# Kernel tuning notes

Measured on AMD Instinct MI355X. Metric: run time of the kernel, lower is better.

Reference implementation:

```python
import jax, jax.numpy as jnp
import numpy as np

B, S, D_IN, D_OUT = 4, 2048, 1024, 1024

def setup_inputs() -> dict:
    key = jax.random.key(0)
    k_x, k_q, k_k, k_v = jax.random.split(key, 4)
    return {
        "x": jax.random.normal(k_x, (B, S, D_IN), dtype=jnp.float32),
        "W_query": jax.random.uniform(k_q, (D_IN, D_OUT), dtype=jnp.float32),
        "W_key": jax.random.uniform(k_k, (D_IN, D_OUT), dtype=jnp.float32),
        "W_value": jax.random.uniform(k_v, (D_IN, D_OUT), dtype=jnp.float32),
    }

def reference(x, W_query, W_key, W_value):
    seq_len = x.shape[1]
    d_out = W_key.shape[-1]
    # fused QKV projection: x @ concat([Wq, Wk, Wv], -1), then split
    qkv = x @ jnp.concatenate([W_query, W_key, W_value], axis=-1)  # [B,S,3*d_out]
    query, key, value = jnp.split(qkv, 3, axis=2)
    # raw scores [B,S,S]; causal mask applied BEFORE scaling (as in source)
    attn_weights = jnp.einsum("bqd,bkd->bqk", query, key)
    causal = jnp.triu(jnp.ones((seq_len, seq_len), dtype=bool), k=1)
    attn_weights = jnp.where(causal[None, :, :], -jnp.inf, attn_weights)
    scaled = attn_weights / jnp.asarray(d_out, x.dtype) ** 0.5
    attn_scores = jax.nn.softmax(scaled, axis=-1)  # dropout p=0 -> identity
    context_vectors = jnp.einsum("bqk,bkd->bqd", attn_scores, value)
    return (context_vectors, attn_scores)
```

## Files before the change

kernel.cpp:

```cpp
#include <hip/hip_runtime.h>
#include <cstdint>
#include <cstddef>


#define S_LEN 2048
#define D_DIM 1024
#define NBATCH 4
#define MEG (1024 * 1024)

typedef __attribute__((ext_vector_type(4))) float floatx4;
typedef __attribute__((ext_vector_type(8))) __bf16 bf16x8;
typedef __attribute__((ext_vector_type(8))) short short8v;

__device__ __forceinline__ unsigned short f2bf(float f) {
  union { float f; unsigned u; } v; v.f = f;
  unsigned r = v.u + 0x7FFF + ((v.u >> 16) & 1);
  return (unsigned short)(r >> 16);
}
__device__ __forceinline__ float bf2f(unsigned short h) {
  union { unsigned u; float f; } v; v.u = ((unsigned)h) << 16; return v.f;
}

__device__ __forceinline__ void async_copy16(const void* g, void* l) {
  __builtin_amdgcn_global_load_lds(
      (const __attribute__((address_space(1))) void*)g,
      (__attribute__((address_space(3))) void*)l, 16, 0, 0);
}

#define VMCNT0() asm volatile("s_waitcnt vmcnt(0)" ::: "memory")
#define RAW_BAR() __builtin_amdgcn_s_barrier()
#define MFMA_BF16 __builtin_amdgcn_mfma_f32_16x16x32_bf16


__device__ __forceinline__ void split_core8(
    const short* __restrict__ Ah, const short* __restrict__ Al,
    const short* __restrict__ Bh, const short* __restrict__ Bl,
    int lda, int ldb, int kIters, int blockM, int blockN,
    short (*AsH)[256][32], short (*AsL)[256][32],
    short (*BsH)[128][32], short (*BsL)[128][32],
    floatx4 (&acc)[4][4])
{
  const int tid  = threadIdx.x;
  const int lane = tid & 63;
  const int wave = tid >> 6;
  const int wm = (wave >> 1) * 64;
  const int wn = (wave & 1) * 64;
  const int fm = lane & 15;
  const int fu = lane >> 4;

  int rA[4], sA[4], rB[4], sB[4];
  #pragma unroll
  for (int i = 0; i < 4; ++i) {
    rA[i] = wm + i * 16 + fm;
    sA[i] = (fu ^ ((rA[i] >> 1) & 3)) * 8;
    rB[i] = wn + i * 16 + fm;
    sB[i] = (fu ^ ((rB[i] >> 1) & 3)) * 8;
  }

  floatx4 zero = {0.f, 0.f, 0.f, 0.f};
  #pragma unroll
  for (int i = 0; i < 4; ++i)
    #pragma unroll
    for (int j = 0; j < 4; ++j)
      acc[i][j] = zero;

  const int r0 = tid >> 2;
  const int u0 = tid & 3;
  const int su = (u0 ^ ((r0 >> 1) & 3)) * 8;
  const size_t a0 = (size_t)(blockM + r0) * lda + su;
  const size_t a1 = a0 + (size_t)128 * lda;
  const size_t b0 = (size_t)(blockN + r0) * ldb + su;

  auto stage0 = [&](int bf, int kb) {
    async_copy16(Ah + a0 + kb, &AsH[bf][r0][u0 * 8]);
    async_copy16(Al + a0 + kb, &AsL[bf][r0][u0 * 8]);
    async_copy16(Bh + b0 + kb, &BsH[bf][r0][u0 * 8]);
  };
  auto stage1 = [&](int bf, int kb) {
    async_copy16(Ah + a1 + kb, &AsH[bf][r0 + 128][u0 * 8]);
    async_copy16(Al + a1 + kb, &AsL[bf][r0 + 128][u0 * 8]);
    async_copy16(Bl + b0 + kb, &BsL[bf][r0][u0 * 8]);
  };

  stage0(0, 0);
  stage1(0, 0);
  VMCNT0();
  RAW_BAR();

  for (int kt = 0; kt < kIters; ++kt) {
    const int cur = kt & 1;
    const int kb = (kt + 1) * 32;
    const bool pf = (kt + 1) < kIters;

    bf16x8 bh[4], bl[4];
    #pragma unroll
    for (int j = 0; j < 4; ++j) {
      bh[j] = *(const bf16x8*)(&BsH[cur][rB[j]][sB[j]]);
      bl[j] = *(const bf16x8*)(&BsL[cur][rB[j]][sB[j]]);
    }
    bf16x8 ah0 = *(const bf16x8*)(&AsH[cur][rA[0]][sA[0]]);
    bf16x8 al0 = *(const bf16x8*)(&AsL[cur][rA[0]][sA[0]]);
    bf16x8 ah1 = *(const bf16x8*)(&AsH[cur][rA[1]][sA[1]]);
    bf16x8 al1 = *(const bf16x8*)(&AsL[cur][rA[1]][sA[1]]);
    if (pf) stage0(cur ^ 1, kb);
    RAW_BAR();
    __builtin_amdgcn_s_setprio(1);
    #pragma unroll
    for (int j = 0; j < 4; ++j) {
      acc[0][j] = MFMA_BF16(ah0, bh[j], acc[0][j], 0, 0, 0);
      acc[0][j] = MFMA_BF16(ah0, bl[j], acc[0][j], 0, 0, 0);
      acc[0][j] = MFMA_BF16(al0, bh[j], acc[0][j], 0, 0, 0);
      acc[1][j] = MFMA_BF16(ah1, bh[j], acc[1][j], 0, 0, 0);
      acc[1][j] = MFMA_BF16(ah1, bl[j], acc[1][j], 0, 0, 0);
      acc[1][j] = MFMA_BF16(al1, bh[j], acc[1][j], 0, 0, 0);
    }
    __builtin_amdgcn_s_setprio(0);
    RAW_BAR();

    bf16x8 ah2 = *(const bf16x8*)(&AsH[cur][rA[2]][sA[2]]);
    bf16x8 al2 = *(const bf16x8*)(&AsL[cur][rA[2]][sA[2]]);
    bf16x8 ah3 = *(const bf16x8*)(&AsH[cur][rA[3]][sA[3]]);
    bf16x8 al3 = *(const bf16x8*)(&AsL[cur][rA[3]][sA[3]]);
    if (pf) stage1(cur ^ 1, kb);
    RAW_BAR();
    __builtin_amdgcn_s_setprio(1);
    #pragma unroll
    for (int j = 0; j < 4; ++j) {
      acc[2][j] = MFMA_BF16(ah2, bh[j], acc[2][j], 0, 0, 0);
      acc[2][j] = MFMA_BF16(ah2, bl[j], acc[2][j], 0, 0, 0);
      acc[2][j] = MFMA_BF16(al2, bh[j], acc[2][j], 0, 0, 0);
      acc[3][j] = MFMA_BF16(ah3, bh[j], acc[3][j], 0, 0, 0);
      acc[3][j] = MFMA_BF16(ah3, bl[j], acc[3][j], 0, 0, 0);
      acc[3][j] = MFMA_BF16(al3, bh[j], acc[3][j], 0, 0, 0);
    }
    __builtin_amdgcn_s_setprio(0);
    VMCNT0();
    RAW_BAR();
  }
}

__device__ __forceinline__ void single_core8(
    const short* __restrict__ A, const short* __restrict__ B,
    int lda, int ldb, int kIters, int blockM, int blockN,
    short (*As)[256][32], short (*Bs)[128][32], floatx4 (&acc)[4][4])
{
  const int tid  = threadIdx.x;
  const int lane = tid & 63;
  const int wave = tid >> 6;
  const int wm = (wave >> 1) * 64;
  const int wn = (wave & 1) * 64;
  const int fm = lane & 15;
  const int fu = lane >> 4;

  int rA[4], sA[4], rB[4], sB[4];
  #pragma unroll
  for (int i = 0; i < 4; ++i) {
    rA[i] = wm + i * 16 + fm;
    sA[i] = (fu ^ ((rA[i] >> 1) & 3)) * 8;
    rB[i] = wn + i * 16 + fm;
    sB[i] = (fu ^ ((rB[i] >> 1) & 3)) * 8;
  }

  floatx4 zero = {0.f, 0.f, 0.f, 0.f};
  #pragma unroll
  for (int i = 0; i < 4; ++i)
    #pragma unroll
    for (int j = 0; j < 4; ++j)
      acc[i][j] = zero;

  const int r0 = tid >> 2;
  const int u0 = tid & 3;
  const int su = (u0 ^ ((r0 >> 1) & 3)) * 8;
  const size_t a0 = (size_t)(blockM + r0) * lda + su;
  const size_t a1 = a0 + (size_t)128 * lda;
  const size_t b0 = (size_t)(blockN + r0) * ldb + su;

  auto stage0 = [&](int bf, int kb) {
    async_copy16(A + a0 + kb, &As[bf][r0][u0 * 8]);
    async_copy16(B + b0 + kb, &Bs[bf][r0][u0 * 8]);
  };
  auto stage1 = [&](int bf, int kb) {
    async_copy16(A + a1 + kb, &As[bf][r0 + 128][u0 * 8]);
  };

  stage0(0, 0);
  stage1(0, 0);
  VMCNT0();
  RAW_BAR();

  for (int kt = 0; kt < kIters; ++kt) {
    const int cur = kt & 1;
    const int kb = (kt + 1) * 32;
    const bool pf = (kt + 1) < kIters;

    bf16x8 bfr[4];
    #pragma unroll
    for (int j = 0; j < 4; ++j)
      bfr[j] = *(const bf16x8*)(&Bs[cur][rB[j]][sB[j]]);
    bf16x8 a0f = *(const bf16x8*)(&As[cur][rA[0]][sA[0]]);
    bf16x8 a1f = *(const bf16x8*)(&As[cur][rA[1]][sA[1]]);
    if (pf) stage0(cur ^ 1, kb);
    RAW_BAR();
    __builtin_amdgcn_s_setprio(1);
    #pragma unroll
    for (int j = 0; j < 4; ++j) {
      acc[0][j] = MFMA_BF16(a0f, bfr[j], acc[0][j], 0, 0, 0);
      acc[1][j] = MFMA_BF16(a1f, bfr[j], acc[1][j], 0, 0, 0);
    }
    __builtin_amdgcn_s_setprio(0);
    RAW_BAR();

    bf16x8 a2f = *(const bf16x8*)(&As[cur][rA[2]][sA[2]]);
    bf16x8 a3f = *(const bf16x8*)(&As[cur][rA[3]][sA[3]]);
    if (pf) stage1(cur ^ 1, kb);
    RAW_BAR();
    __builtin_amdgcn_s_setprio(1);
    #pragma unroll
    for (int j = 0; j < 4; ++j) {
      acc[2][j] = MFMA_BF16(a2f, bfr[j], acc[2][j], 0, 0, 0);
      acc[3][j] = MFMA_BF16(a3f, bfr[j], acc[3][j], 0, 0, 0);
    }
    __builtin_amdgcn_s_setprio(0);
    VMCNT0();
    RAW_BAR();
  }
}


__global__ __launch_bounds__(256) void k_cvt_w(
    const float* __restrict__ wq, const float* __restrict__ wk,
    const float* __restrict__ wv,
    short* __restrict__ wqh, short* __restrict__ wql,
    short* __restrict__ wkh, short* __restrict__ wkl,
    short* __restrict__ wvt, float* __restrict__ muSum,
    int* __restrict__ cnt)
{
  const int bid = blockIdx.x;
  const int tid = threadIdx.x;
  if (bid < 1024) {
    const float4* src;
    short *dh, *dl;
    size_t idx;
    if (bid < 512) {
      idx = (size_t)bid * 256 + tid;
      src = (const float4*)wq; dh = wqh; dl = wql;
    } else {
      idx = (size_t)(bid - 512) * 256 + tid;
      src = (const float4*)wk; dh = wkh; dl = wkl;
    }
    const float4 u4 = src[idx * 2];
    const float4 w4 = src[idx * 2 + 1];
    float f[8] = {u4.x, u4.y, u4.z, u4.w, w4.x, w4.y, w4.z, w4.w};
    short8v oh, ol;
    #pragma unroll
    for (int e = 0; e < 8; ++e) {
      const unsigned short h = f2bf(f[e]);
      oh[e] = (short)h;
      ol[e] = (short)f2bf(f[e] - bf2f(h));
    }
    *(short8v*)(dh + idx * 8) = oh;
    *(short8v*)(dl + idx * 8) = ol;
  } else {
    if (bid == 1024) {
      float4 z = {0.f, 0.f, 0.f, 0.f};
      ((float4*)muSum)[tid] = z;
      if (tid == 0) *cnt = 0;
    }
    const int rem = bid - 1024;
    const int bx = rem & 31, by = rem >> 5;
    const int tx = tid & 31, ty = tid >> 5;
    __shared__ float tile[32][33];
    const int colIn = bx * 32 + tx;
    #pragma unroll
    for (int i = 0; i < 4; ++i) {
      const int rowIn = by * 32 + ty + i * 8;
      tile[ty + i * 8][tx] = wv[(size_t)rowIn * D_DIM + colIn];
    }
    __syncthreads();
    const int colOut = by * 32 + tx;
    #pragma unroll
    for (int i = 0; i < 4; ++i) {
      const int rowOut = bx * 32 + ty + i * 8;
      wvt[(size_t)rowOut * D_DIM + colOut] = (short)f2bf(tile[tx][ty + i * 8]);
    }
  }
}


__global__ __launch_bounds__(256) void k_m_cvtx(
    const short* __restrict__ wqh, const short* __restrict__ wql,
    const short* __restrict__ wkh, const short* __restrict__ wkl,
    short* __restrict__ mth, short* __restrict__ mtl,
    float* __restrict__ muSum,
    const float4* __restrict__ x,
    short* __restrict__ xh, short* __restrict__ xl)
{
  __shared__ alignas(16) short AsH[2][64][32];
  __shared__ alignas(16) short AsL[2][64][32];
  __shared__ alignas(16) short BsH[2][64][32];
  __shared__ alignas(16) short BsL[2][64][32];
  const int g = blockIdx.x;
  const int tid = threadIdx.x;

  if (g < 256) {
    floatx4 acc[2][2];
    const int blockM = (g >> 4) * 64;
    const int blockN = (g & 15) * 64;
    const int lane = tid & 63, wave = tid >> 6;
    const int wm = (wave >> 1) * 32, wn = (wave & 1) * 32;
    const int fm = lane & 15, fk = (lane >> 4) * 8;

    floatx4 zero = {0.f, 0.f, 0.f, 0.f};
    #pragma unroll
    for (int i = 0; i < 2; ++i)
      #pragma unroll
      for (int j = 0; j < 2; ++j)
        acc[i][j] = zero;

    const int sr = tid >> 2;
    const int sc = (tid & 3) * 8;
    const short* ah0 = wkh + (size_t)(blockM + sr) * D_DIM + sc;
    const short* al0 = wkl + (size_t)(blockM + sr) * D_DIM + sc;
    const short* bh0 = wqh + (size_t)(blockN + sr) * D_DIM + sc;
    const short* bl0 = wql + (size_t)(blockN + sr) * D_DIM + sc;
    short* ahB = &AsH[0][0][0]; short* alB = &AsL[0][0][0];
    short* bhB = &BsH[0][0][0]; short* blB = &BsL[0][0][0];
    const int l0 = tid * 8, l1 = (tid + 256) * 8;

    for (int kt = 0; kt < 16; ++kt) {
      const int kb = kt * 64;
      async_copy16(ah0 + kb, ahB + l0);
      async_copy16(ah0 + kb + 32, ahB + l1);
      async_copy16(al0 + kb, alB + l0);
      async_copy16(al0 + kb + 32, alB + l1);
      async_copy16(bh0 + kb, bhB + l0);
      async_copy16(bh0 + kb + 32, bhB + l1);
      async_copy16(bl0 + kb, blB + l0);
      async_copy16(bl0 + kb + 32, blB + l1);
      __syncthreads();
      #pragma unroll
      for (int ks = 0; ks < 2; ++ks) {
        bf16x8 ah[2], al[2], bh[2], bl[2];
        #pragma unroll
        for (int i = 0; i < 2; ++i) {
          ah[i] = *(const bf16x8*)(&AsH[ks][wm + i * 16 + fm][fk]);
          al[i] = *(const bf16x8*)(&AsL[ks][wm + i * 16 + fm][fk]);
        }
        #pragma unroll
        for (int j = 0; j < 2; ++j) {
          bh[j] = *(const bf16x8*)(&BsH[ks][wn + j * 16 + fm][fk]);
          bl[j] = *(const bf16x8*)(&BsL[ks][wn + j * 16 + fm][fk]);
        }
        #pragma unroll
        for (int i = 0; i < 2; ++i)
          #pragma unroll
          for (int j = 0; j < 2; ++j) {
            acc[i][j] = MFMA_BF16(ah[i], bh[j], acc[i][j], 0, 0, 0);
            acc[i][j] = MFMA_BF16(ah[i], bl[j], acc[i][j], 0, 0, 0);
            acc[i][j] = MFMA_BF16(al[i], bh[j], acc[i][j], 0, 0, 0);
          }
      }
      __syncthreads();
    }

    const int rb = wm + ((lane >> 4) << 2);
    const int cb = wn + (lane & 15);
    #pragma unroll
    for (int i = 0; i < 2; ++i)
      #pragma unroll
      for (int j = 0; j < 2; ++j) {
        const int n = blockN + cb + j * 16;
        #pragma unroll
        for (int r = 0; r < 2 * 2; ++r) {
          const int m = blockM + rb + i * 16 + r;
          const float f = acc[i][j][r];
          const unsigned short h = f2bf(f);
          mth[(size_t)m * D_DIM + n] = (short)h;
          mtl[(size_t)m * D_DIM + n] = (short)f2bf(f - bf2f(h));
        }
      }
    #pragma unroll
    for (int i = 0; i < 2; ++i)
      #pragma unroll
      for (int r = 0; r < 4; ++r) {
        float v = acc[i][0][r] + acc[i][1][r];
        v += __shfl_xor(v, 1); v += __shfl_xor(v, 2);
        v += __shfl_xor(v, 4); v += __shfl_xor(v, 8);
        if ((lane & 15) == 0)
          atomicAdd(&muSum[blockM + rb + i * 16 + r], v);
      }
  } else {
    const size_t idx = (size_t)(g - 256) * 256 + tid;
    const float4 u4 = x[idx * 2];
    const float4 w4 = x[idx * 2 + 1];
    float f[8] = {u4.x, u4.y, u4.z, u4.w, w4.x, w4.y, w4.z, w4.w};
    short8v oh, ol;
    #pragma unroll
    for (int e = 0; e < 8; ++e) {
      const unsigned short h = f2bf(f[e]);
      oh[e] = (short)h;
      ol[e] = (short)f2bf(f[e] - bf2f(h));
    }
    *(short8v*)(xh + idx * 8) = oh;
    *(short8v*)(xl + idx * 8) = ol;
  }
}


__global__ __launch_bounds__(256) void k_rowstats(
    const short* __restrict__ xh, const short* __restrict__ xl,
    const float* __restrict__ muSum, float* __restrict__ sq, float* __restrict__ u)
{
  const int r = blockIdx.x, tid = threadIdx.x;
  const ushort4 h = *(const ushort4*)(xh + (size_t)r * D_DIM + tid * 4);
  const ushort4 l = *(const ushort4*)(xl + (size_t)r * D_DIM + tid * 4);
  const float4 m4 = *(const float4*)(muSum + tid * 4);
  const float x0 = bf2f(h.x) + bf2f(l.x);
  const float x1 = bf2f(h.y) + bf2f(l.y);
  const float x2 = bf2f(h.z) + bf2f(l.z);
  const float x3 = bf2f(h.w) + bf2f(l.w);
  float s = x0 + x1 + x2 + x3;
  float uu = m4.x * x0 + m4.y * x1 + m4.z * x2 + m4.w * x3;
  #pragma unroll
  for (int off = 32; off > 0; off >>= 1) {
    s  += __shfl_xor(s, off);
    uu += __shfl_xor(uu, off);
  }
  __shared__ float ps[4], pu[4];
  if ((tid & 63) == 0) { ps[tid >> 6] = s; pu[tid >> 6] = uu; }
  __syncthreads();
  if (tid == 0) {
    sq[r] = ps[0] + ps[1] + ps[2] + ps[3];
    u[r]  = (pu[0] + pu[1] + pu[2] + pu[3]) * (1.0f / 1024.0f);
  }
}


__global__ __launch_bounds__(512) void k_gemm_n8(
    const short* __restrict__ xh, const short* __restrict__ xl,
    const short* __restrict__ mth, const short* __restrict__ mtl,
    const float* __restrict__ sq, const float* __restrict__ muSum,
    short* __restrict__ nh, short* __restrict__ nl)
{
  __shared__ alignas(16) short AsH[2][256][32];
  __shared__ alignas(16) short AsL[2][256][32];
  __shared__ alignas(16) short BsH[2][128][32];
  __shared__ alignas(16) short BsL[2][128][32];
  floatx4 acc[4][4];
  const int g = blockIdx.x;
  const int swz = (g & 7) * 32 + (g >> 3);
  const int blockM = (swz >> 3) * 256;
  const int blockN = (swz & 7) * 128;
  split_core8(xh, xl, mth, mtl, D_DIM, D_DIM, D_DIM / 32,
              blockM, blockN, AsH, AsL, BsH, BsL, acc);

  const int tid = threadIdx.x, lane = tid & 63, wave = tid >> 6;
  const int wm = (wave >> 1) * 64, wn = (wave & 1) * 64;
  const int rb = wm + ((lane >> 4) << 2);
  const int cb = wn + (lane & 15);
  #pragma unroll
  for (int i = 0; i < 4; ++i)
    #pragma unroll
    for (int j = 0; j < 4; ++j) {
      const int n = blockN + cb + j * 16;
      const float muv = muSum[n] * (1.0f / 1024.0f);
      #pragma unroll
      for (int r = 0; r < 4; ++r) {
        const int m = blockM + rb + i * 16 + r;
        const float f = acc[i][j][r] - sq[m] * muv;
        const unsigned short h = f2bf(f);
        nh[(size_t)m * D_DIM + n] = (short)h;
        nl[(size_t)m * D_DIM + n] = (short)f2bf(f - bf2f(h));
      }
    }
}


__global__ __launch_bounds__(512) void k_gemm_sv8(
    const short* __restrict__ nh, const short* __restrict__ nl,
    const short* __restrict__ xh, const short* __restrict__ xl,
    const float* __restrict__ sq, const float* __restrict__ u,
    const short* __restrict__ wvt, float* __restrict__ attn,
    short* __restrict__ vt, int* __restrict__ cnt)
{
  __shared__ alignas(16) short AsH[2][256][32];
  __shared__ alignas(16) short AsL[2][256][32];
  __shared__ alignas(16) short BsH[2][128][32];
  __shared__ alignas(16) short BsL[2][128][32];
  __shared__ int s_item;

  const int tid = threadIdx.x, lane = tid & 63, wave = tid >> 6;
  const int wm = (wave >> 1) * 64, wn = (wave & 1) * 64;
  const int rb = wm + ((lane >> 4) << 2);
  const int cb = wn + (lane & 15);

  for (;;) {
    if (tid == 0) s_item = atomicAdd(cnt, 1);
    __syncthreads();
    const int item = s_item;
    if (item >= 544) return;

    floatx4 acc[4][4];
    if (item < 288) {
      const int b = item / 72;
      int t = item - b * 72;
      int bi = 0;
      while (t >= 2 * bi + 2) { t -= 2 * bi + 2; ++bi; }
      const int bj = t;

      const size_t boff = (size_t)b * S_LEN * D_DIM;
      split_core8(nh + boff, nl + boff, xh + boff, xl + boff,
                  D_DIM, D_DIM, D_DIM / 32, bi * 256, bj * 128,
                  AsH, AsL, BsH, BsL, acc);

      float* out = attn + (size_t)b * S_LEN * S_LEN;
      const int rowBase = (b << 11) + bi * 256;
      const int colBase = (b << 11) + bj * 128;
      #pragma unroll
      for (int j = 0; j < 4; ++j) {
        const int n = bj * 128 + cb + j * 16;
        const float uv = u[colBase + cb + j * 16];
        #pragma unroll
        for (int i = 0; i < 4; ++i)
          #pragma unroll
          for (int r = 0; r < 4; ++r) {
            const int m = bi * 256 + rb + i * 16 + r;
            const float sv = sq[rowBase + rb + i * 16 + r];
            out[(size_t)m * S_LEN + n] = acc[i][j][r] + sv * uv;
          }
      }
    } else {
      const int vb = item - 288;
      const int blockM = (vb >> 3) * 256;
      const int blockN = (vb & 7) * 128;
      single_core8(xh, wvt, D_DIM, D_DIM, D_DIM / 32, blockM, blockN,
                   AsH, BsH, acc);
      #pragma unroll
      for (int i = 0; i < 4; ++i)
        #pragma unroll
        for (int j = 0; j < 4; ++j) {
          const int n = blockN + cb + j * 16;
          const int m0 = blockM + rb + i * 16;
          const int b = m0 >> 11;
          const int s0 = m0 & (S_LEN - 1);
          ushort4 pk;
          pk.x = f2bf(acc[i][j][0]); pk.y = f2bf(acc[i][j][1]);
          pk.z = f2bf(acc[i][j][2]); pk.w = f2bf(acc[i][j][3]);
          *(ushort4*)(vt + ((size_t)b * D_DIM + n) * S_LEN + s0) = pk;
        }
    }
  }
}


__global__ __launch_bounds__(256) void k_softmax(float* __restrict__ attn,
                                                 short* __restrict__ pb) {
  const int b = blockIdx.x >> 11;
  const int q = blockIdx.x & (S_LEN - 1);
  float* row  = attn + ((size_t)b * S_LEN + q) * S_LEN;
  short* prow = pb   + ((size_t)b * S_LEN + q) * S_LEN;
  const int tid = threadIdx.x;
  const int k0 = tid * 8;
  const int kBand = ((q >> 7) + 1) << 7;
  __shared__ float sMax[4], sSum[4];

  float v[8];
  if (k0 <= q) {
    const float4 a0 = *(const float4*)(row + k0);
    const float4 a1 = *(const float4*)(row + k0 + 4);
    v[0] = a0.x; v[1] = a0.y; v[2] = a0.z; v[3] = a0.w;
    v[4] = a1.x; v[5] = a1.y; v[6] = a1.z; v[7] = a1.w;
  } else {
    #pragma unroll
    for (int e = 0; e < 8; ++e) v[e] = -3.0e38f;
  }

  float mx = -3.0e38f;
  #pragma unroll
  for (int e = 0; e < 8; ++e) {
    v[e] = (k0 + e <= q) ? v[e] : -3.0e38f;
    mx = fmaxf(mx, v[e]);
  }
  #pragma unroll
  for (int off = 32; off > 0; off >>= 1) mx = fmaxf(mx, __shfl_xor(mx, off));
  if ((tid & 63) == 0) sMax[tid >> 6] = mx;
  __syncthreads();
  mx = fmaxf(fmaxf(sMax[0], sMax[1]), fmaxf(sMax[2], sMax[3]));

  float s = 0.f;
  #pragma unroll
  for (int e = 0; e < 8; ++e) {
    const float p = (k0 + e <= q) ? __expf((v[e] - mx) * 0.03125f) : 0.f;
    v[e] = p;
    s += p;
  }
  #pragma unroll
  for (int off = 32; off > 0; off >>= 1) s += __shfl_xor(s, off);
  if ((tid & 63) == 0) sSum[tid >> 6] = s;
  __syncthreads();
  s = sSum[0] + sSum[1] + sSum[2] + sSum[3];
  const float inv = 1.0f / s;

  float o[8];
  #pragma unroll
  for (int e = 0; e < 8; ++e) o[e] = v[e] * inv;
  float4 w0 = {o[0], o[1], o[2], o[3]};
  float4 w1 = {o[4], o[5], o[6], o[7]};
  *(float4*)(row + k0) = w0;
  *(float4*)(row + k0 + 4) = w1;
  if (k0 < kBand) {
    ushort4 p0, p1;
    p0.x = f2bf(o[0]); p0.y = f2bf(o[1]); p0.z = f2bf(o[2]); p0.w = f2bf(o[3]);
    p1.x = f2bf(o[4]); p1.y = f2bf(o[5]); p1.z = f2bf(o[6]); p1.w = f2bf(o[7]);
    *(ushort4*)(prow + k0) = p0;
    *(ushort4*)(prow + k0 + 4) = p1;
  }
}


__global__ __launch_bounds__(256) void k_gemm_ctx(
    const short* __restrict__ pb, const short* __restrict__ vt,
    float* __restrict__ ctx)
{
  __shared__ alignas(16) short As2[2][128][32];
  __shared__ alignas(16) short Bs2[2][128][32];
  floatx4 acc[4][4];
  const int b = blockIdx.z;
  const int by = 15 - blockIdx.y;
  const int blockM = by * 128;
  const int blockN = blockIdx.x * 128;
  const int kIters = (by + 1) * 2;
  const short* A = pb + (size_t)b * S_LEN * S_LEN;
  const short* B = vt + (size_t)b * D_DIM * S_LEN;

  const int tid = threadIdx.x, lane = tid & 63, wave = tid >> 6;
  const int wm = (wave >> 1) * 64, wn = (wave & 1) * 64;
  const int fm = lane & 15, fk = (lane >> 4) * 8;
  const int r0 = tid >> 2, c0 = (tid & 3) * 8;

  floatx4 zero = {0.f, 0.f, 0.f, 0.f};
  #pragma unroll
  for (int i = 0; i < 4; ++i)
    #pragma unroll
    for (int j = 0; j < 4; ++j)
      acc[i][j] = zero;

  const short* a0 = A + (size_t)(blockM + r0) * S_LEN + c0;
  const short* a1 = a0 + (size_t)64 * S_LEN;
  const short* b0 = B + (size_t)(blockN + r0) * S_LEN + c0;
  const short* b1 = b0 + (size_t)64 * S_LEN;
  short* asBase = &As2[0][0][0];
  short* bsBase = &Bs2[0][0][0];
  short* as0 = asBase + (size_t)tid * 8;
  short* as1 = asBase + (size_t)(tid + 256) * 8;
  short* as2 = asBase + (size_t)(tid + 512) * 8;
  short* as3 = asBase + (size_t)(tid + 768) * 8;
  short* bs0 = bsBase + (size_t)tid * 8;
  short* bs1 = bsBase + (size_t)(tid + 256) * 8;
  short* bs2 = bsBase + (size_t)(tid + 512) * 8;
  short* bs3 = bsBase + (size_t)(tid + 768) * 8;

  for (int kt = 0; kt < kIters; ++kt) {
    const int kb = kt * 64;
    async_copy16(a0 + kb, as0);
    async_copy16(a1 + kb, as1);
    async_copy16(a0 + kb + 32, as2);
    async_copy16(a1 + kb + 32, as3);
    async_copy16(b0 + kb, bs0);
    async_copy16(b1 + kb, bs1);
    async_copy16(b0 + kb + 32, bs2);
    async_copy16(b1 + kb + 32, bs3);
    __syncthreads();
    #pragma unroll
    for (int ks = 0; ks < 2; ++ks) {
      bf16x8 af[4], bfr[4];
      #pragma unroll
      for (int i = 0; i < 4; ++i)
        af[i] = *(const bf16x8*)(&As2[ks][wm + i * 16 + fm][fk]);
      #pragma unroll
      for (int j = 0; j < 4; ++j)
        bfr[j] = *(const bf16x8*)(&Bs2[ks][wn + j * 16 + fm][fk]);
      #pragma unroll
      for (int i = 0; i < 4; ++i)
        #pragma unroll
        for (int j = 0; j < 4; ++j)
          acc[i][j] = MFMA_BF16(af[i], bfr[j], acc[i][j], 0, 0, 0);
    }
    __syncthreads();
  }

  float* out = ctx + (size_t)b * S_LEN * D_DIM;
  const int rb = wm + ((lane >> 4) << 2);
  const int cb = wn + (lane & 15);
  #pragma unroll
  for (int i = 0; i < 4; ++i)
    #pragma unroll
    for (int j = 0; j < 4; ++j) {
      const int n = blockN + cb + j * 16;
      #pragma unroll
      for (int r = 0; r < 4; ++r) {
        const int m = blockM + rb + i * 16 + r;
        out[(size_t)m * D_DIM + n] = acc[i][j][r];
      }
    }
}


extern "C" void kernel_launch(void* const* d_in, const int* in_sizes, int n_in,
                              void* d_out, int out_size, void* d_ws, size_t ws_size,
                              hipStream_t stream) {
  const float* x  = (const float*)d_in[0];
  const float* wq = (const float*)d_in[1];
  const float* wk = (const float*)d_in[2];
  const float* wv = (const float*)d_in[3];

  float* out  = (float*)d_out;
  float* ctx  = out;
  float* attn = out + (size_t)NBATCH * S_LEN * D_DIM;

  short* ws  = (short*)d_ws;
  short* xh  = ws;
  short* xl  = xh + (size_t)8 * MEG;
  short* wqh = xl + (size_t)8 * MEG;
  short* wql = wqh + (size_t)1 * MEG;
  short* wkh = wql + (size_t)1 * MEG;
  short* wkl = wkh + (size_t)1 * MEG;
  short* wvt = wkl + (size_t)1 * MEG;
  short* mth = wvt + (size_t)1 * MEG;
  short* mtl = mth + (size_t)1 * MEG;
  short* nh  = mtl + (size_t)1 * MEG;
  short* nl  = nh + (size_t)8 * MEG;
  short* vt  = nl + (size_t)8 * MEG;
  short* pb  = nh;
  float* fb  = (float*)(vt + (size_t)8 * MEG);
  float* muS = fb;
  float* sq  = fb + 1024;
  float* u   = sq + 8192;
  int*   cnt = (int*)(u + 8192);

  k_cvt_w<<<2048, 256, 0, stream>>>(wq, wk, wv, wqh, wql, wkh, wkl, wvt,
                                    muS, cnt);
  k_m_cvtx<<<4352, 256, 0, stream>>>(wqh, wql, wkh, wkl, mth, mtl, muS,
                                     (const float4*)x, xh, xl);
  k_rowstats<<<8192, 256, 0, stream>>>(xh, xl, muS, sq, u);
  k_gemm_n8<<<256, 512, 0, stream>>>(xh, xl, mth, mtl, sq, muS, nh, nl);
  k_gemm_sv8<<<256, 512, 0, stream>>>(nh, nl, xh, xl, sq, u, wvt, attn,
                                      vt, cnt);
  k_softmax<<<NBATCH * S_LEN, 256, 0, stream>>>(attn, pb);
  k_gemm_ctx<<<dim3(8, 16, 4), 256, 0, stream>>>(pb, vt, ctx);
}
```

Measured before the change: 360.4 us.

## Single-buffer LDS in score/V GEMM kernel and double its persistent grid

The persistent scores/V-projection kernel now uses single-buffered shared-memory tiles instead of double buffers, which halves its LDS footprint, and its grid grows from 256 to 512 blocks. The aim is to fit two blocks per CU so that one block's loads can overlap with another's MFMA work, replacing the software prefetch pipeline inside each block. The cost is that each block now stalls on the full load before every k-step, and register pressure from loading all A/B fragments at once may limit the occupancy gain.

Measured after the change: 376.4 us. +4.4%, slower.

```diff
diff --git a/kernel.cpp b/kernel.cpp
--- a/kernel.cpp
+++ b/kernel.cpp
@@ -32,7 +32,7 @@
 #define MFMA_BF16 __builtin_amdgcn_mfma_f32_16x16x32_bf16
 
 
-__device__ __forceinline__ void split_core8(
+__device__ __forceinline__ void split_core8_db(
     const short* __restrict__ Ah, const short* __restrict__ Al,
     const short* __restrict__ Bh, const short* __restrict__ Bl,
     int lda, int ldb, int kIters, int blockM, int blockN,
@@ -139,10 +139,13 @@
   }
 }
 
-__device__ __forceinline__ void single_core8(
-    const short* __restrict__ A, const short* __restrict__ B,
+__device__ __forceinline__ void split_core8_sb(
+    const short* __restrict__ Ah, const short* __restrict__ Al,
+    const short* __restrict__ Bh, const short* __restrict__ Bl,
     int lda, int ldb, int kIters, int blockM, int blockN,
-    short (*As)[256][32], short (*Bs)[128][32], floatx4 (&acc)[4][4])
+    short (*AsH)[32], short (*AsL)[32],
+    short (*BsH)[32], short (*BsL)[32],
+    floatx4 (&acc)[4][4])
 {
   const int tid  = threadIdx.x;
   const int lane = tid & 63;
@@ -175,54 +178,100 @@
   const size_t a1 = a0 + (size_t)128 * lda;
   const size_t b0 = (size_t)(blockN + r0) * ldb + su;
 
-  auto stage0 = [&](int bf, int kb) {
-    async_copy16(A + a0 + kb, &As[bf][r0][u0 * 8]);
-    async_copy16(B + b0 + kb, &Bs[bf][r0][u0 * 8]);
-  };
-  auto stage1 = [&](int bf, int kb) {
-    async_copy16(A + a1 + kb, &As[bf][r0 + 128][u0 * 8]);
-  };
-
-  stage0(0, 0);
-  stage1(0, 0);
-  VMCNT0();
-  RAW_BAR();
-
   for (int kt = 0; kt < kIters; ++kt) {
-    const int cur = kt & 1;
-    const int kb = (kt + 1) * 32;
-    const bool pf = (kt + 1) < kIters;
-
-    bf16x8 bfr[4];
+    const int kb = kt * 32;
+    async_copy16(Ah + a0 + kb, &AsH[r0][u0 * 8]);
+    async_copy16(Al + a0 + kb, &AsL[r0][u0 * 8]);
+    async_copy16(Bh + b0 + kb, &BsH[r0][u0 * 8]);
+    async_copy16(Ah + a1 + kb, &AsH[r0 + 128][u0 * 8]);
+    async_copy16(Al + a1 + kb, &AsL[r0 + 128][u0 * 8]);
+    async_copy16(Bl + b0 + kb, &BsL[r0][u0 * 8]);
+    __syncthreads();
+
+    bf16x8 bh[4], bl[4], ah[4], al[4];
+    #pragma unroll
+    for (int j = 0; j < 4; ++j) {
+      bh[j] = *(const bf16x8*)(&BsH[rB[j]][sB[j]]);
+      bl[j] = *(const bf16x8*)(&BsL[rB[j]][sB[j]]);
+    }
+    #pragma unroll
+    for (int i = 0; i < 4; ++i) {
+      ah[i] = *(const bf16x8*)(&AsH[rA[i]][sA[i]]);
+      al[i] = *(const bf16x8*)(&AsL[rA[i]][sA[i]]);
+    }
+    __builtin_amdgcn_s_setprio(1);
+    #pragma unroll
+    for (int i = 0; i < 4; ++i)
+      #pragma unroll
+      for (int j = 0; j < 4; ++j) {
+        acc[i][j] = MFMA_BF16(ah[i], bh[j], acc[i][j], 0, 0, 0);
+        acc[i][j] = MFMA_BF16(ah[i], bl[j], acc[i][j], 0, 0, 0);
+        acc[i][j] = MFMA_BF16(al[i], bh[j], acc[i][j], 0, 0, 0);
+      }
+    __builtin_amdgcn_s_setprio(0);
+    __syncthreads();
+  }
+}
+
+__device__ __forceinline__ void single_core8_sb(
+    const short* __restrict__ A, const short* __restrict__ B,
+    int lda, int ldb, int kIters, int blockM, int blockN,
+    short (*As)[32], short (*Bs)[32], floatx4 (&acc)[4][4])
+{
+  const int tid  = threadIdx.x;
+  const int lane = tid & 63;
+  const int wave = tid >> 6;
+  const int wm = (wave >> 1) * 64;
+  const int wn = (wave & 1) * 64;
+  const int fm = lane & 15;
+  const int fu = lane >> 4;
+
+  int rA[4], sA[4], rB[4], sB[4];
+  #pragma unroll
+  for (int i = 0; i < 4; ++i) {
+    rA[i] = wm + i * 16 + fm;
+    sA[i] = (fu ^ ((rA[i] >> 1) & 3)) * 8;
+    rB[i] = wn + i * 16 + fm;
+    sB[i] = (fu ^ ((rB[i] >> 1) & 3)) * 8;
+  }
+
+  floatx4 zero = {0.f, 0.f, 0.f, 0.f};
+  #pragma unroll
+  for (int i = 0; i < 4; ++i)
     #pragma unroll
     for (int j = 0; j < 4; ++j)
-      bfr[j] = *(const bf16x8*)(&Bs[cur][rB[j]][sB[j]]);
-    bf16x8 a0f = *(const bf16x8*)(&As[cur][rA[0]][sA[0]]);
-    bf16x8 a1f = *(const bf16x8*)(&As[cur][rA[1]][sA[1]]);
-    if (pf) stage0(cur ^ 1, kb);
-    RAW_BAR();
+      acc[i][j] = zero;
+
+  const int r0 = tid >> 2;
+  const int u0 = tid & 3;
+  const int su = (u0 ^ ((r0 >> 1) & 3)) * 8;
+  const size_t a0 = (size_t)(blockM + r0) * lda + su;
+  const size_t a1 = a0 + (size_t)128 * lda;
+  const size_t b0 = (size_t)(blockN + r0) * ldb + su;
+
+  for (int kt = 0; kt < kIters; ++kt) {
+    const int kb = kt * 32;
+    async_copy16(A + a0 + kb, &As[r0][u0 * 8]);
+    async_copy16(B + b0 + kb, &Bs[r0][u0 * 8]);
+    async_copy16(A + a1 + kb, &As[r0 + 128][u0 * 8]);
+    __syncthreads();
+
+    bf16x8 bfr[4], af[4];
+    #pragma unroll
+    for (int j = 0; j < 4; ++j)
+      bfr[j] = *(const bf16x8*)(&Bs[rB[j]][sB[j]]);
+    #pragma unroll
+    for (int i = 0; i < 4; ++i)
+      af[i] = *(const bf16x8*)(&As[rA[i]][sA[i]]);
+
     __builtin_amdgcn_s_setprio(1);
     #pragma unroll
-    for (int j = 0; j < 4; ++j) {
-      acc[0][j] = MFMA_BF16(a0f, bfr[j], acc[0][j], 0, 0, 0);
-      acc[1][j] = MFMA_BF16(a1f, bfr[j], acc[1][j], 0, 0, 0);
-    }
+    for (int i = 0; i < 4; ++i)
+      #pragma unroll
+      for (int j = 0; j < 4; ++j)
+        acc[i][j] = MFMA_BF16(af[i], bfr[j], acc[i][j], 0, 0, 0);
     __builtin_amdgcn_s_setprio(0);
-    RAW_BAR();
-
-    bf16x8 a2f = *(const bf16x8*)(&As[cur][rA[2]][sA[2]]);
-    bf16x8 a3f = *(const bf16x8*)(&As[cur][rA[3]][sA[3]]);
-    if (pf) stage1(cur ^ 1, kb);
-    RAW_BAR();
-    __builtin_amdgcn_s_setprio(1);
-    #pragma unroll
-    for (int j = 0; j < 4; ++j) {
-      acc[2][j] = MFMA_BF16(a2f, bfr[j], acc[2][j], 0, 0, 0);
-      acc[3][j] = MFMA_BF16(a3f, bfr[j], acc[3][j], 0, 0, 0);
-    }
-    __builtin_amdgcn_s_setprio(0);
-    VMCNT0();
-    RAW_BAR();
+    __syncthreads();
   }
 }
 
@@ -451,8 +500,8 @@
   const int swz = (g & 7) * 32 + (g >> 3);
   const int blockM = (swz >> 3) * 256;
   const int blockN = (swz & 7) * 128;
-  split_core8(xh, xl, mth, mtl, D_DIM, D_DIM, D_DIM / 32,
-              blockM, blockN, AsH, AsL, BsH, BsL, acc);
+  split_core8_db(xh, xl, mth, mtl, D_DIM, D_DIM, D_DIM / 32,
+                 blockM, blockN, AsH, AsL, BsH, BsL, acc);
 
   const int tid = threadIdx.x, lane = tid & 63, wave = tid >> 6;
   const int wm = (wave >> 1) * 64, wn = (wave & 1) * 64;
@@ -483,10 +532,10 @@
     const short* __restrict__ wvt, float* __restrict__ attn,
     short* __restrict__ vt, int* __restrict__ cnt)
 {
-  __shared__ alignas(16) short AsH[2][256][32];
-  __shared__ alignas(16) short AsL[2][256][32];
-  __shared__ alignas(16) short BsH[2][128][32];
-  __shared__ alignas(16) short BsL[2][128][32];
+  __shared__ alignas(16) short AsH[256][32];
+  __shared__ alignas(16) short AsL[256][32];
+  __shared__ alignas(16) short BsH[128][32];
+  __shared__ alignas(16) short BsL[128][32];
   __shared__ int s_item;
 
   const int tid = threadIdx.x, lane = tid & 63, wave = tid >> 6;
@@ -509,9 +558,9 @@
       const int bj = t;
 
       const size_t boff = (size_t)b * S_LEN * D_DIM;
-      split_core8(nh + boff, nl + boff, xh + boff, xl + boff,
-                  D_DIM, D_DIM, D_DIM / 32, bi * 256, bj * 128,
-                  AsH, AsL, BsH, BsL, acc);
+      split_core8_sb(nh + boff, nl + boff, xh + boff, xl + boff,
+                     D_DIM, D_DIM, D_DIM / 32, bi * 256, bj * 128,
+                     AsH, AsL, BsH, BsL, acc);
 
       float* out = attn + (size_t)b * S_LEN * S_LEN;
       const int rowBase = (b << 11) + bi * 256;
@@ -533,8 +582,8 @@
       const int vb = item - 288;
       const int blockM = (vb >> 3) * 256;
       const int blockN = (vb & 7) * 128;
-      single_core8(xh, wvt, D_DIM, D_DIM, D_DIM / 32, blockM, blockN,
-                   AsH, BsH, acc);
+      single_core8_sb(xh, wvt, D_DIM, D_DIM, D_DIM / 32, blockM, blockN,
+                      AsH, BsH, acc);
       #pragma unroll
       for (int i = 0; i < 4; ++i)
         #pragma unroll
@@ -744,7 +793,7 @@
                                      (const float4*)x, xh, xl);
   k_rowstats<<<8192, 256, 0, stream>>>(xh, xl, muS, sq, u);
   k_gemm_n8<<<256, 512, 0, stream>>>(xh, xl, mth, mtl, sq, muS, nh, nl);
-  k_gemm_sv8<<<256, 512, 0, stream>>>(nh, nl, xh, xl, sq, u, wvt, attn,
+  k_gemm_sv8<<<512, 512, 0, stream>>>(nh, nl, xh, xl, sq, u, wvt, attn,
                                       vt, cnt);
   k_softmax<<<NBATCH * S_LEN, 256, 0, stream>>>(attn, pb);
   k_gemm_ctx<<<dim3(8, 16, 4), 256, 0, stream>>>(pb, vt, ctx);
```
